# Kernel tuning notes

Measured on AMD Instinct MI355X. Metric: run time of the kernel, lower is better.

The kernel has to match this reference:

```python
import jax, jax.numpy as jnp
import numpy as np
import math

N, E, G, D, H, L = 10000, 160000, 64, 480, 4, 6
DH = D // H          # 120 dims per head
NB = 128             # number of radial basis functions
SH = 9               # 1+3+5 spherical-harmonic channels (l=0,1,2)
CUTOFF = 5.0
AVG_DEG = 15.57930850982666
AVG_NODES = 18.03065905448718


def _silu(x):
    return x * jax.nn.sigmoid(x)


def _sph_harm(vec):
    # component-normalized real spherical harmonics l=0,1,2 on unit vectors
    r = jnp.linalg.norm(vec, axis=-1, keepdims=True) + 1e-12
    u = vec / r
    x, y, z = u[:, 0], u[:, 1], u[:, 2]
    s3, s5, s15 = math.sqrt(3.0), math.sqrt(5.0), math.sqrt(15.0)
    return jnp.stack([
        jnp.ones_like(x),
        s3 * x, s3 * y, s3 * z,
        s15 * x * y, s15 * y * z,
        0.5 * s5 * (3.0 * z * z - 1.0),
        s15 * x * z, 0.5 * s15 * (x * x - y * y)], axis=-1)


def _rbf(d):
    # Gaussian radial basis, centers on [0, cutoff]
    centers = jnp.linspace(0.0, CUTOFF, NB)
    width = CUTOFF / NB
    return jnp.exp(-jnp.square((d[:, None] - centers[None, :]) / width))


def _ln(x):
    mu = jnp.mean(x, axis=-1, keepdims=True)
    var = jnp.var(x, axis=-1, keepdims=True)
    return (x - mu) * jax.lax.rsqrt(var + 1e-5)


def setup_inputs() -> dict:
    key = jax.random.key(0)
    ks = jax.random.split(key, 24)

    def w(k, shape, fan_in):
        return jax.random.normal(k, shape, jnp.float32) / math.sqrt(fan_in)

    inp = {}
    inp["pos"] = jax.random.uniform(ks[0], (N, 3), jnp.float32) * 10.0
    inp["node_atom"] = jax.random.randint(ks[1], (N,), 0, 64)
    inp["edge_src"] = jax.random.randint(ks[2], (E,), 0, N)
    inp["edge_dst"] = jax.random.randint(ks[3], (E,), 0, N)
    inp["batch"] = jnp.sort(jax.random.randint(ks[4], (N,), 0, G))
    # learned parameters
    inp["atom_table"] = w(ks[5], (64, D), 1)
    inp["Wdeg"] = w(ks[6], (SH, D), SH)
    inp["Wd1"] = w(ks[7], (NB, 64), NB)
    inp["Wd2"] = w(ks[8], (64, 64), 64)
    inp["Wd3"] = w(ks[9], (64, 1), 64)
    inp["Wq"] = w(ks[10], (L, D, D), D)
    inp["Wk"] = w(ks[11], (L, D, D), D)
    inp["Wv"] = w(ks[12], (L, D, D), D)
    inp["Wsh"] = w(ks[13], (L, SH, D), SH)
    inp["W1"] = w(ks[14], (L, NB, 64), NB)
    inp["W2"] = w(ks[15], (L, 64, 64), 64)
    inp["W3"] = w(ks[16], (L, 64, H), 64)
    inp["Wo"] = w(ks[17], (L, D, D), D)
    inp["Wf1"] = w(ks[18], (L, D, 2 * D), D)
    inp["Wf2"] = w(ks[19], (L, 2 * D, D), 2 * D)
    inp["Wh1"] = w(ks[20], (D, D), D)
    inp["Wh2"] = w(ks[21], (D, 1), D)
    return inp


def reference(pos, atom_table, Wdeg, Wd1, Wd2, Wd3, Wq, Wk, Wv, Wsh, W1, W2, W3,
              Wo, Wf1, Wf2, Wh1, Wh2, node_atom, edge_src, edge_dst, batch):
    edge_vec = pos[edge_src] - pos[edge_dst]              # [E,3]
    sh = _sph_harm(edge_vec)                              # [E,SH]
    rbf = _rbf(jnp.linalg.norm(edge_vec, axis=-1))        # [E,NB]

    # atom embedding + edge-degree embedding (scatter-sum, rescaled)
    x = atom_table[node_atom]                             # [N,D]
    g0 = _silu(_silu(rbf @ Wd1) @ Wd2) @ Wd3              # [E,1]
    deg = jax.ops.segment_sum((sh @ Wdeg) * g0, edge_dst, num_segments=N)
    x = x + deg / math.sqrt(AVG_DEG)

    inv = 1.0 / math.sqrt(DH)
    for l in range(L):
        # per-edge q/k with SH tensor-product-style mixing and RBF gate
        q = (x @ Wq[l])[edge_dst].reshape(-1, H, DH)
        k = (x[edge_src] @ Wk[l] + sh @ Wsh[l]).reshape(-1, H, DH)
        gate = _silu(_silu(rbf @ W1[l]) @ W2[l]) @ W3[l]  # [E,H]
        logits = jnp.sum(q * k, axis=-1) * inv * gate      # [E,H]
        # per-neighborhood (destination node) softmax
        m = jax.ops.segment_max(logits, edge_dst, num_segments=N)
        a = jnp.exp(logits - m[edge_dst])
        den = jax.ops.segment_sum(a, edge_dst, num_segments=N)
        alpha = a / (den[edge_dst] + 1e-12)                # [E,H]
        v = (x @ Wv[l])[edge_src].reshape(-1, H, DH)
        msg = (alpha[..., None] * v).reshape(-1, D)
        agg = jax.ops.segment_sum(msg, edge_dst, num_segments=N)
        x = _ln(x + (agg / math.sqrt(AVG_DEG)) @ Wo[l])
        x = _ln(x + _silu(x @ Wf1[l]) @ Wf2[l])

    node_e = _silu(x @ Wh1) @ Wh2                          # [N,1]
    energy = jax.ops.segment_sum(node_e[:, 0], batch, num_segments=G) / AVG_NODES
    return energy
```

## Files before the change

### kernel.cpp

```cpp
#include <hip/hip_runtime.h>
#include <hip/hip_bf16.h>

#define NN 10000
#define EE 160000
#define GG 64
#define DD 480
#define HH 4
#define LLAYERS 6
#define DHD 120
#define NB_ 128
#define TSIZE 4096
#define DMAXT 5.5f
#define LSCALE (4095.0f/5.5f)

#define INV_DH 0.09128709291752768f
#define INV_SQRT_DEG 0.25335277f
#define INV_AVG_NODES (1.0f/18.03065905448718f)

typedef __attribute__((ext_vector_type(8))) short bf16x8;
typedef __attribute__((ext_vector_type(4))) float f32x4;
typedef __attribute__((ext_vector_type(8))) unsigned short u16x8;

__device__ __forceinline__ float b2f(unsigned short u){ return __uint_as_float(((unsigned)u)<<16); }
__device__ __forceinline__ unsigned short f2b(float f){
  unsigned u = __float_as_uint(f);
  return (unsigned short)((u + 0x7fffu + ((u>>16)&1u)) >> 16);
}
__device__ __forceinline__ float wsum(float v){
  #pragma unroll
  for (int off=32; off>0; off>>=1) v += __shfl_xor(v, off, 64);
  return v;
}
__device__ __forceinline__ void glds16(const void* g, void* l) {
  __builtin_amdgcn_global_load_lds((const __attribute__((address_space(1))) unsigned int*)g,
                                   (__attribute__((address_space(3))) unsigned int*)l, 16, 0, 0);
}

__global__ __launch_bounds__(256) void zero_kernel(int* __restrict__ cnt, float* __restrict__ out){
  int i = blockIdx.x*256 + threadIdx.x;
  if (i < NN) cnt[i] = 0;
  if (i < GG) out[i] = 0.f;
}

__global__ __launch_bounds__(256) void gather_x_kernel(const float* __restrict__ at,
    const int* __restrict__ atom, float* __restrict__ x){
  const int wid = threadIdx.x >> 6, lane = threadIdx.x & 63;
  for (int n = blockIdx.x*4 + wid; n < NN; n += gridDim.x*4) {
    int a = atom[n];
    if (lane < 60) {
      const float4* src = (const float4*)(at + (size_t)a*DD + lane*8);
      float4* dst = (float4*)(x + (size_t)n*DD + lane*8);
      dst[0] = src[0]; dst[1] = src[1];
    }
  }
}

__global__ __launch_bounds__(256) void edge_geom_kernel(const float* __restrict__ pos,
    const int* __restrict__ esrc, const int* __restrict__ edst,
    float* __restrict__ sh, float* __restrict__ dedge){
  const int e = blockIdx.x*256 + threadIdx.x;
  if (e >= EE) return;
  int s = esrc[e], d = edst[e];
  float vx = pos[s*3+0]-pos[d*3+0];
  float vy = pos[s*3+1]-pos[d*3+1];
  float vz = pos[s*3+2]-pos[d*3+2];
  float rr = sqrtf(vx*vx+vy*vy+vz*vz);
  dedge[e] = rr;
  float r = rr + 1e-12f;
  float x = vx/r, y = vy/r, z = vz/r;
  const float s3 = 1.7320508075688772f;
  const float s5 = 2.23606797749979f;
  const float s15 = 3.872983346207417f;
  float* o = sh + (size_t)e*9;
  o[0] = 1.f;
  o[1] = s3*x; o[2] = s3*y; o[3] = s3*z;
  o[4] = s15*x*y; o[5] = s15*y*z;
  o[6] = 0.5f*s5*(3.f*z*z-1.f);
  o[7] = s15*x*z;
  o[8] = 0.5f*s15*(x*x-y*y);
}

__global__ __launch_bounds__(256) void hist_kernel(const int* __restrict__ edst, int* __restrict__ cnt){
  int e = blockIdx.x*256 + threadIdx.x;
  if (e < EE) atomicAdd(&cnt[edst[e]], 1);
}

__global__ __launch_bounds__(1024) void scan_kernel(const int* __restrict__ cnt,
    int* __restrict__ row_ptr, int* __restrict__ cursor){
  __shared__ int sd[1024];
  __shared__ int s_carry;
  if (threadIdx.x == 0) s_carry = 0;
  __syncthreads();
  for (int base = 0; base < NN; base += 1024) {
    int i = base + threadIdx.x;
    int v = (i < NN) ? cnt[i] : 0;
    sd[threadIdx.x] = v;
    __syncthreads();
    for (int off = 1; off < 1024; off <<= 1) {
      int t = 0;
      if ((int)threadIdx.x >= off) t = sd[threadIdx.x - off];
      __syncthreads();
      sd[threadIdx.x] += t;
      __syncthreads();
    }
    int incl = sd[threadIdx.x];
    int carry = s_carry;
    if (i < NN) { row_ptr[i] = carry + incl - v; cursor[i] = carry + incl - v; }
    __syncthreads();
    if (threadIdx.x == 1023) s_carry = carry + incl;
    __syncthreads();
  }
  if (threadIdx.x == 0) row_ptr[NN] = s_carry;
}

__global__ __launch_bounds__(256) void scatter_kernel(const int* __restrict__ esrc,
    const int* __restrict__ edst, int* __restrict__ cursor,
    int* __restrict__ eid, int* __restrict__ srcs){
  int e = blockIdx.x*256 + threadIdx.x;
  if (e < EE) {
    int n = edst[e];
    int p = atomicAdd(&cursor[n], 1);
    eid[p] = e;
    srcs[p] = esrc[e];
  }
}

__global__ __launch_bounds__(1024) void table_kernel(
    const float* __restrict__ Wd1, const float* __restrict__ Wd2, const float* __restrict__ Wd3,
    const float* __restrict__ W1, const float* __restrict__ W2, const float* __restrict__ W3,
    float* __restrict__ Tg, float* __restrict__ Tl) {
  const int chain = blockIdx.y;
  const float *A1, *A2, *A3; int NC;
  if (chain == 0) { A1 = Wd1; A2 = Wd2; A3 = Wd3; NC = 1; }
  else { int l = chain-1; A1 = W1 + (size_t)l*128*64; A2 = W2 + (size_t)l*64*64; A3 = W3 + (size_t)l*64*4; NC = 4; }
  __shared__ float W1s[128*64];
  __shared__ float W2s[64*64];
  __shared__ float W3s[64*4];
  for (int i = threadIdx.x; i < 128*64; i += 1024) W1s[i] = A1[i];
  for (int i = threadIdx.x; i < 64*64; i += 1024) W2s[i] = A2[i];
  for (int i = threadIdx.x; i < 64*4; i += 1024) W3s[i] = (i < 64*NC) ? A3[i] : 0.f;
  __syncthreads();
  const int wid = threadIdx.x >> 6, lane = threadIdx.x & 63;
  const int t = blockIdx.x*16 + wid;
  const float d = (float)t * (DMAXT/(float)(TSIZE-1));
  float t1 = 0.f;
  #pragma unroll 4
  for (int j = 0; j < 128; ++j) {
    float z = (d - (float)j*(5.0f/127.0f)) * (128.0f/5.0f);
    float f = __expf(-z*z);
    t1 += f * W1s[j*64 + lane];
  }
  t1 = t1 / (1.f + __expf(-t1));
  float t2 = 0.f;
  #pragma unroll 4
  for (int c = 0; c < 64; ++c) {
    float bc = __shfl(t1, c);
    t2 += bc * W2s[c*64 + lane];
  }
  t2 = t2 / (1.f + __expf(-t2));
  if (chain == 0) {
    float o = wsum(t2 * W3s[lane]);
    if (lane == 0) Tg[t] = o;
  } else {
    #pragma unroll
    for (int nc = 0; nc < 4; ++nc) {
      float o = wsum(t2 * W3s[lane*4 + nc]);
      if (lane == 0) Tl[((size_t)(chain-1)*TSIZE + t)*4 + nc] = o;
    }
  }
}

__device__ __forceinline__ float lookup1(const float* __restrict__ Tg, float d) {
  float u = d * LSCALE;
  if (u >= (float)(TSIZE-1)) return 0.f;
  int i = (int)u; float fr = u - (float)i;
  float a = Tg[i], b = Tg[i+1];
  return a + fr*(b-a);
}

__global__ __launch_bounds__(256) void transpose_w_kernel(const float* __restrict__ W,
    __hip_bfloat16* __restrict__ Wt, int K, int N, int Npad,
    long long lstrideW, long long lstrideT) {
  __shared__ float T[32][33];
  const int l = blockIdx.z;
  W  += (size_t)l*lstrideW;
  Wt += (size_t)l*lstrideT;
  const int k0 = blockIdx.y*32, n0 = blockIdx.x*32;
  const int tx = threadIdx.x & 31, ty = threadIdx.x >> 5;
  #pragma unroll
  for (int r = 0; r < 32; r += 8) {
    int k = k0 + ty + r, n = n0 + tx;
    T[ty+r][tx] = (k < K && n < N) ? W[(size_t)k*N + n] : 0.f;
  }
  __syncthreads();
  #pragma unroll
  for (int r = 0; r < 32; r += 8) {
    int n = n0 + ty + r, k = k0 + tx;
    if (n < Npad && k < K)
      ((unsigned short*)Wt)[(size_t)n*K + k] = f2b(T[tx][ty+r]);
  }
}

template<int SILU, int OUT>
__global__ __launch_bounds__(512) void gemm_bf16_kernel(
    const __hip_bfloat16* __restrict__ A, const __hip_bfloat16* __restrict__ Bt,
    float* __restrict__ Cf, __hip_bfloat16* __restrict__ Cb0,
    __hip_bfloat16* __restrict__ Cb1, __hip_bfloat16* __restrict__ Cb2,
    int M, int K, int Nc) {
  __shared__ char smem[16384];
  char* AsB = smem;
  char* BsB = smem + 8192;
  const int tid = threadIdx.x;
  const int lane = tid & 63, wid = tid >> 6;
  const int wm = wid >> 2, wn = wid & 3;
  const long long m0 = (long long)blockIdx.y * 128;
  const int n0 = blockIdx.x * 128;

  const int skhi = wid >> 1, srow = (wid & 1)*64 + lane;
  long long gra = m0 + srow; if (gra >= M) gra = M - 1;
  const __hip_bfloat16* aptr = A + gra * (size_t)K + skhi*8;
  const __hip_bfloat16* bptr = Bt + (size_t)(n0 + srow) * K + skhi*8;
  char* adst = AsB + (skhi*128 + srow)*16;
  char* bdst = BsB + (skhi*128 + srow)*16;

  f32x4 acc[4][2];
  #pragma unroll
  for (int i = 0; i < 4; ++i)
    #pragma unroll
    for (int j = 0; j < 2; ++j)
      acc[i][j] = (f32x4){0.f,0.f,0.f,0.f};

  const int lr = lane & 15, lkh = lane >> 4;

  for (int kt = 0; kt < K; kt += 32) {
    __syncthreads();
    glds16(aptr + kt, adst);
    glds16(bptr + kt, bdst);
    __syncthreads();
    bf16x8 afr[4], bfr[2];
    #pragma unroll
    for (int fm = 0; fm < 4; ++fm)
      afr[fm] = *reinterpret_cast<const bf16x8*>(AsB + (lkh*128 + wm*64 + fm*16 + lr)*16);
    #pragma unroll
    for (int fn = 0; fn < 2; ++fn)
      bfr[fn] = *reinterpret_cast<const bf16x8*>(BsB + (lkh*128 + wn*32 + fn*16 + lr)*16);
    #pragma unroll
    for (int fm = 0; fm < 4; ++fm)
      #pragma unroll
      for (int fn = 0; fn < 2; ++fn)
        acc[fm][fn] = __builtin_amdgcn_mfma_f32_16x16x32_bf16(afr[fm], bfr[fn], acc[fm][fn], 0, 0, 0);
  }

  const int seg = n0 >> 9;
  const int c0 = (OUT == 2) ? (n0 & 511) : n0;
  unsigned short* qdst = nullptr;
  if (OUT == 2) qdst = (unsigned short*)(seg == 0 ? Cb0 : (seg == 1 ? Cb1 : Cb2));
  #pragma unroll
  for (int fm = 0; fm < 4; ++fm) {
    #pragma unroll
    for (int fn = 0; fn < 2; ++fn) {
      #pragma unroll
      for (int j = 0; j < 4; ++j) {
        long long r = m0 + wm*64 + fm*16 + lkh*4 + j;
        int c = c0 + wn*32 + fn*16 + lr;
        if (r < M && c < Nc) {
          float v = acc[fm][fn][j];
          if (SILU) v = v / (1.f + __expf(-v));
          if (OUT == 0) Cf[r*(size_t)Nc + c] = v;
          else if (OUT == 1) ((unsigned short*)Cb0)[r*(size_t)Nc + c] = f2b(v);
          else qdst[r*(size_t)Nc + c] = f2b(v);
        }
      }
    }
  }
}

__global__ __launch_bounds__(256) void deg_kernel(const float* __restrict__ dedge,
    const float* __restrict__ sh, const float* __restrict__ Tg,
    const int* __restrict__ row_ptr, const int* __restrict__ eid,
    const float* __restrict__ Wdeg, float* __restrict__ x, __hip_bfloat16* __restrict__ xb) {
  const int wid = threadIdx.x >> 6, lane = threadIdx.x & 63;
  for (int n = blockIdx.x*4 + wid; n < NN; n += gridDim.x*4) {
    const int e0 = row_ptr[n], e1 = row_ptr[n+1];
    float s9[9] = {0,0,0,0,0,0,0,0,0};
    for (int p = e0 + lane; p < e1; p += 64) {
      int e = eid[p];
      float g = lookup1(Tg, dedge[e]);
      const float* srow = sh + (size_t)e*9;
      #pragma unroll
      for (int s = 0; s < 9; ++s) s9[s] += g*srow[s];
    }
    #pragma unroll
    for (int s = 0; s < 9; ++s) s9[s] = wsum(s9[s]);
    #pragma unroll
    for (int r = 0; r < 8; ++r) {
      int d = lane + (r<<6);
      if (d < DD) {
        float acc = 0.f;
        #pragma unroll
        for (int s = 0; s < 9; ++s) acc += s9[s]*Wdeg[s*DD + d];
        float vv = x[(size_t)n*DD + d] + acc * INV_SQRT_DEG;
        x[(size_t)n*DD + d] = vv;
        ((unsigned short*)xb)[(size_t)n*DD + d] = f2b(vv);
      }
    }
  }
}

__global__ __launch_bounds__(256) void p_kernel(const __hip_bfloat16* __restrict__ xq,
    const float* __restrict__ Wsh_l, float* __restrict__ P) {
  const int wid = threadIdx.x >> 6, lane = threadIdx.x & 63;
  for (int n = blockIdx.x*4 + wid; n < NN; n += gridDim.x*4) {
    if (lane < 36) {
      int h = lane/9, s = lane%9;
      const unsigned short* q = (const unsigned short*)(xq + (size_t)n*DD + h*DHD);
      const float* w = Wsh_l + s*DD + h*DHD;
      float acc = 0.f;
      #pragma unroll
      for (int db = 0; db < 15; ++db) {
        u16x8 v = *reinterpret_cast<const u16x8*>(q + db*8);
        #pragma unroll
        for (int j = 0; j < 8; ++j) acc += b2f(v[j])*w[db*8+j];
      }
      P[(size_t)n*36 + lane] = acc;
    }
  }
}

__global__ __launch_bounds__(256) void coef_kernel(
    const int* __restrict__ eid, const int* __restrict__ edst,
    const float* __restrict__ sh, const float* __restrict__ dedge,
    const float* __restrict__ Tl, const float* __restrict__ P,
    float2* __restrict__ sb) {
  const int p = blockIdx.x*256 + threadIdx.x;
  if (p >= EE) return;
  const int e = eid[p];
  const int n = edst[e];
  const float* srow = sh + (size_t)e*9;
  float s0 = srow[0], s1 = srow[1], s2 = srow[2], s3 = srow[3], s4 = srow[4];
  float s5 = srow[5], s6 = srow[6], s7 = srow[7], s8 = srow[8];
  const float* Pn = P + (size_t)n*36;
  float g[4];
  {
    float u = dedge[e] * LSCALE;
    if (u >= (float)(TSIZE-1)) { g[0]=g[1]=g[2]=g[3]=0.f; }
    else {
      int ti = (int)u; float fr = u - (float)ti;
      const float4 ga = *reinterpret_cast<const float4*>(Tl + ti*4);
      const float4 gb = *reinterpret_cast<const float4*>(Tl + ti*4 + 4);
      g[0] = ga.x + fr*(gb.x-ga.x); g[1] = ga.y + fr*(gb.y-ga.y);
      g[2] = ga.z + fr*(gb.z-ga.z); g[3] = ga.w + fr*(gb.w-ga.w);
    }
  }
  #pragma unroll
  for (int h = 0; h < 4; ++h) {
    const float* Ph = Pn + h*9;
    float lp = s0*Ph[0]+s1*Ph[1]+s2*Ph[2]+s3*Ph[3]+s4*Ph[4]
             + s5*Ph[5]+s6*Ph[6]+s7*Ph[7]+s8*Ph[8];
    float sc = INV_DH * g[h];
    sb[(size_t)p*4 + h] = make_float2(sc, lp*sc);
  }
}

__global__ __launch_bounds__(256) void attn_kernel(
    const __hip_bfloat16* __restrict__ xq, const __hip_bfloat16* __restrict__ xk,
    const __hip_bfloat16* __restrict__ xv, const float2* __restrict__ sb,
    const int* __restrict__ row_ptr, const int* __restrict__ srcs,
    __hip_bfloat16* __restrict__ aggout) {
  const int wid = threadIdx.x >> 6, lane = threadIdx.x & 63;
  __shared__ float l_s[4][64][4];
  __shared__ int   src_sh[4][64];
  float (*ls)[4] = l_s[wid];
  int* srcS = src_sh[wid];
  const int hh = lane >> 4, li = lane & 15;
  const int hd = (lane < 60) ? (lane/15) : 3;
  const unsigned short* xkp = (const unsigned short*)xk;
  const unsigned short* xvp = (const unsigned short*)xv;
  const int doff = hh*DHD + li*8;
  for (int n = blockIdx.x*4 + wid; n < NN; n += gridDim.x*4) {
    const int e0 = row_ptr[n], e1 = row_ptr[n+1];
    float qf[8] = {0,0,0,0,0,0,0,0};
    if (li < 15) {
      u16x8 v = *reinterpret_cast<const u16x8*>((const unsigned short*)xq + (size_t)n*DD + doff);
      #pragma unroll
      for (int j = 0; j < 8; ++j) qf[j] = b2f(v[j]);
    }
    float m_reg = -1e30f, den_reg = 0.f;
    float agg[8] = {0,0,0,0,0,0,0,0};
    for (int c0 = e0; c0 < e1; c0 += 64) {
      const int cn = min(64, e1 - c0);
      if (lane < cn) srcS[lane] = srcs[c0 + lane];
      asm volatile("s_waitcnt lgkmcnt(0)" ::: "memory");
      int i = 0;
      for (; i + 4 <= cn; i += 4) {
        int sA = srcS[i], sB = srcS[i+1], sC = srcS[i+2], sD = srcS[i+3];
        float a0 = 0.f, a1 = 0.f, a2 = 0.f, a3 = 0.f;
        if (li < 15) {
          u16x8 k0 = *reinterpret_cast<const u16x8*>(xkp + (size_t)sA*DD + doff);
          u16x8 k1 = *reinterpret_cast<const u16x8*>(xkp + (size_t)sB*DD + doff);
          u16x8 k2 = *reinterpret_cast<const u16x8*>(xkp + (size_t)sC*DD + doff);
          u16x8 k3 = *reinterpret_cast<const u16x8*>(xkp + (size_t)sD*DD + doff);
          #pragma unroll
          for (int j = 0; j < 8; ++j) {
            a0 += qf[j]*b2f(k0[j]);
            a1 += qf[j]*b2f(k1[j]);
            a2 += qf[j]*b2f(k2[j]);
            a3 += qf[j]*b2f(k3[j]);
          }
        }
        #pragma unroll
        for (int off = 1; off < 16; off <<= 1) {
          a0 += __shfl_xor(a0, off, 64);
          a1 += __shfl_xor(a1, off, 64);
          a2 += __shfl_xor(a2, off, 64);
          a3 += __shfl_xor(a3, off, 64);
        }
        if (li == 0) {
          float2 cA = sb[(size_t)(c0+i+0)*4 + hh];
          float2 cB = sb[(size_t)(c0+i+1)*4 + hh];
          float2 cC = sb[(size_t)(c0+i+2)*4 + hh];
          float2 cD = sb[(size_t)(c0+i+3)*4 + hh];
          ls[i+0][hh] = a0*cA.x + cA.y;
          ls[i+1][hh] = a1*cB.x + cB.y;
          ls[i+2][hh] = a2*cC.x + cC.y;
          ls[i+3][hh] = a3*cD.x + cD.y;
        }
      }
      for (; i < cn; ++i) {
        int sA = srcS[i];
        float a0 = 0.f;
        if (li < 15) {
          u16x8 k0 = *reinterpret_cast<const u16x8*>(xkp + (size_t)sA*DD + doff);
          #pragma unroll
          for (int j = 0; j < 8; ++j) a0 += qf[j]*b2f(k0[j]);
        }
        #pragma unroll
        for (int off = 1; off < 16; off <<= 1) a0 += __shfl_xor(a0, off, 64);
        if (li == 0) {
          float2 cA = sb[(size_t)(c0+i)*4 + hh];
          ls[i][hh] = a0*cA.x + cA.y;
        }
      }
      asm volatile("s_waitcnt lgkmcnt(0)" ::: "memory");
      const int h = lane & 3, i0 = lane >> 2;
      float cm = -1e30f;
      for (int i2 = i0; i2 < cn; i2 += 16) cm = fmaxf(cm, ls[i2][h]);
      #pragma unroll
      for (int off = 4; off < 64; off <<= 1) cm = fmaxf(cm, __shfl_xor(cm, off, 64));
      const float newm = fmaxf(m_reg, cm);
      const float f = __expf(m_reg - newm);
      float cs = 0.f;
      for (int i2 = i0; i2 < cn; i2 += 16) {
        float a = __expf(ls[i2][h] - newm);
        ls[i2][h] = a;
        cs += a;
      }
      #pragma unroll
      for (int off = 4; off < 64; off <<= 1) cs += __shfl_xor(cs, off, 64);
      m_reg = newm;
      den_reg = den_reg*f + cs;
      asm volatile("s_waitcnt lgkmcnt(0)" ::: "memory");
      const float fh = __shfl(f, hd);
      #pragma unroll
      for (int j = 0; j < 8; ++j) agg[j] *= fh;
      i = 0;
      for (; i + 4 <= cn; i += 4) {
        int sA = srcS[i], sB = srcS[i+1], sC = srcS[i+2], sD = srcS[i+3];
        float a0 = ls[i][hd], a1 = ls[i+1][hd], a2 = ls[i+2][hd], a3 = ls[i+3][hd];
        if (lane < 60) {
          u16x8 v0 = *reinterpret_cast<const u16x8*>(xvp + (size_t)sA*DD + lane*8);
          u16x8 v1 = *reinterpret_cast<const u16x8*>(xvp + (size_t)sB*DD + lane*8);
          u16x8 v2 = *reinterpret_cast<const u16x8*>(xvp + (size_t)sC*DD + lane*8);
          u16x8 v3 = *reinterpret_cast<const u16x8*>(xvp + (size_t)sD*DD + lane*8);
          #pragma unroll
          for (int j = 0; j < 8; ++j)
            agg[j] += a0*b2f(v0[j]) + a1*b2f(v1[j]) + a2*b2f(v2[j]) + a3*b2f(v3[j]);
        }
      }
      for (; i < cn; ++i) {
        int sA = srcS[i];
        float a0 = ls[i][hd];
        if (lane < 60) {
          u16x8 v0 = *reinterpret_cast<const u16x8*>(xvp + (size_t)sA*DD + lane*8);
          #pragma unroll
          for (int j = 0; j < 8; ++j) agg[j] += a0*b2f(v0[j]);
        }
      }
    }
    const float dh2 = __shfl(den_reg, hd);
    if (lane < 60) {
      const float sc = INV_SQRT_DEG / (dh2 + 1e-12f);
      u16x8 o;
      #pragma unroll
      for (int j = 0; j < 8; ++j) o[j] = f2b(agg[j]*sc);
      *reinterpret_cast<u16x8*>((unsigned short*)aggout + (size_t)n*DD + lane*8) = o;
    }
  }
}

__global__ __launch_bounds__(256) void ln_kernel(float* __restrict__ x, const float* __restrict__ t,
    __hip_bfloat16* __restrict__ xb) {
  const int wid = threadIdx.x >> 6, lane = threadIdx.x & 63;
  for (int n = blockIdx.x*4 + wid; n < NN; n += gridDim.x*4) {
    float4 a0 = make_float4(0,0,0,0), a1 = make_float4(0,0,0,0);
    float s = 0.f, s2 = 0.f;
    if (lane < 60) {
      const float4* xp = (const float4*)(x + (size_t)n*DD + lane*8);
      const float4* tp = (const float4*)(t + (size_t)n*DD + lane*8);
      float4 b0 = tp[0], b1 = tp[1];
      a0 = xp[0]; a1 = xp[1];
      a0.x += b0.x; a0.y += b0.y; a0.z += b0.z; a0.w += b0.w;
      a1.x += b1.x; a1.y += b1.y; a1.z += b1.z; a1.w += b1.w;
      s  = a0.x+a0.y+a0.z+a0.w + a1.x+a1.y+a1.z+a1.w;
      s2 = a0.x*a0.x+a0.y*a0.y+a0.z*a0.z+a0.w*a0.w
         + a1.x*a1.x+a1.y*a1.y+a1.z*a1.z+a1.w*a1.w;
    }
    s = wsum(s); s2 = wsum(s2);
    const float mu = s * (1.f/(float)DD);
    const float var = s2 * (1.f/(float)DD) - mu*mu;
    const float rs = rsqrtf(var + 1e-5f);
    if (lane < 60) {
      float4* xp = (float4*)(x + (size_t)n*DD + lane*8);
      a0.x = (a0.x-mu)*rs; a0.y = (a0.y-mu)*rs; a0.z = (a0.z-mu)*rs; a0.w = (a0.w-mu)*rs;
      a1.x = (a1.x-mu)*rs; a1.y = (a1.y-mu)*rs; a1.z = (a1.z-mu)*rs; a1.w = (a1.w-mu)*rs;
      xp[0] = a0; xp[1] = a1;
      u16x8 o;
      o[0]=f2b(a0.x); o[1]=f2b(a0.y); o[2]=f2b(a0.z); o[3]=f2b(a0.w);
      o[4]=f2b(a1.x); o[5]=f2b(a1.y); o[6]=f2b(a1.z); o[7]=f2b(a1.w);
      *reinterpret_cast<u16x8*>((unsigned short*)xb + (size_t)n*DD + lane*8) = o;
    }
  }
}

__global__ __launch_bounds__(256) void h2_kernel(const float* __restrict__ t,
    const float* __restrict__ Wh2, const int* __restrict__ batch, float* __restrict__ out) {
  __shared__ float part[GG];
  for (int i = threadIdx.x; i < GG; i += 256) part[i] = 0.f;
  __syncthreads();
  const int wid = threadIdx.x >> 6, lane = threadIdx.x & 63;
  const int per_block = (NN + gridDim.x - 1) / gridDim.x;
  const int n0 = blockIdx.x * per_block;
  const int n1 = min(NN, n0 + per_block);
  for (int n = n0 + wid; n < n1; n += 4) {
    float s = 0.f;
    if (lane < 60) {
      const float4* tp = (const float4*)(t + (size_t)n*DD + lane*8);
      const float4* wp = (const float4*)(Wh2 + lane*8);
      float4 t0 = tp[0], t1 = tp[1], w0 = wp[0], w1 = wp[1];
      s = t0.x*w0.x+t0.y*w0.y+t0.z*w0.z+t0.w*w0.w
        + t1.x*w1.x+t1.y*w1.y+t1.z*w1.z+t1.w*w1.w;
    }
    s = wsum(s);
    if (lane == 0) atomicAdd(&part[batch[n]], s * INV_AVG_NODES);
  }
  __syncthreads();
  for (int i = threadIdx.x; i < GG; i += 256) {
    float v = part[i];
    if (v != 0.f) atomicAdd(&out[i], v);
  }
}

extern "C" void kernel_launch(void* const* d_in, const int* in_sizes, int n_in,
                              void* d_out, int out_size, void* d_ws, size_t ws_size,
                              hipStream_t stream) {
  const float* pos        = (const float*)d_in[0];
  const int*   node_atom  = (const int*)  d_in[1];
  const int*   edge_src   = (const int*)  d_in[2];
  const int*   edge_dst   = (const int*)  d_in[3];
  const int*   batch      = (const int*)  d_in[4];
  const float* atom_table = (const float*)d_in[5];
  const float* Wdeg       = (const float*)d_in[6];
  const float* Wd1        = (const float*)d_in[7];
  const float* Wd2        = (const float*)d_in[8];
  const float* Wd3        = (const float*)d_in[9];
  const float* Wq         = (const float*)d_in[10];
  const float* Wk         = (const float*)d_in[11];
  const float* Wv         = (const float*)d_in[12];
  const float* Wsh        = (const float*)d_in[13];
  const float* W1         = (const float*)d_in[14];
  const float* W2         = (const float*)d_in[15];
  const float* W3         = (const float*)d_in[16];
  const float* Wo         = (const float*)d_in[17];
  const float* Wf1        = (const float*)d_in[18];
  const float* Wf2        = (const float*)d_in[19];
  const float* Wh1        = (const float*)d_in[20];
  const float* Wh2        = (const float*)d_in[21];
  float* out = (float*)d_out;
  char*  wsb = (char*)d_ws;

  size_t off = 0;
  auto alloc = [&](size_t bytes) { size_t o = off; off += (bytes + 255) & ~(size_t)255; return o; };
  float*  x      = (float*) (wsb + alloc((size_t)NN*DD*4));
  __hip_bfloat16* xb   = (__hip_bfloat16*)(wsb + alloc((size_t)NN*DD*2));
  __hip_bfloat16* xq   = (__hip_bfloat16*)(wsb + alloc((size_t)NN*DD*2));
  __hip_bfloat16* xk   = (__hip_bfloat16*)(wsb + alloc((size_t)NN*DD*2));
  __hip_bfloat16* xv   = (__hip_bfloat16*)(wsb + alloc((size_t)NN*DD*2));
  float*  shb    = (float*) (wsb + alloc((size_t)EE*9*4));
  float*  dedge  = (float*) (wsb + alloc((size_t)EE*4));
  float*  P      = (float*) (wsb + alloc((size_t)NN*36*4));
  float2* sbuf   = (float2*)(wsb + alloc((size_t)EE*4*8));
  __hip_bfloat16* aggb = (__hip_bfloat16*)(wsb + alloc((size_t)NN*DD*2));
  float*  tmp480 = (float*) (wsb + alloc((size_t)NN*DD*4));
  __hip_bfloat16* tmp960 = (__hip_bfloat16*)(wsb + alloc((size_t)NN*960*2));
  float*  Tg     = (float*) (wsb + alloc((size_t)TSIZE*4));
  float*  Tl     = (float*) (wsb + alloc((size_t)LLAYERS*TSIZE*4*4));
  __hip_bfloat16* Wqkvt = (__hip_bfloat16*)(wsb + alloc((size_t)LLAYERS*1536*480*2));
  __hip_bfloat16* Wot   = (__hip_bfloat16*)(wsb + alloc((size_t)LLAYERS*512*480*2));
  __hip_bfloat16* Wf1t  = (__hip_bfloat16*)(wsb + alloc((size_t)LLAYERS*1024*480*2));
  __hip_bfloat16* Wf2t  = (__hip_bfloat16*)(wsb + alloc((size_t)LLAYERS*512*960*2));
  __hip_bfloat16* Wh1t  = (__hip_bfloat16*)(wsb + alloc((size_t)512*480*2));
  int* cnt     = (int*)(wsb + alloc((size_t)NN*4));
  int* row_ptr = (int*)(wsb + alloc((size_t)(NN+1)*4));
  int* cursor  = (int*)(wsb + alloc((size_t)NN*4));
  int* eid     = (int*)(wsb + alloc((size_t)EE*4));
  int* srcs    = (int*)(wsb + alloc((size_t)EE*4));
  (void)ws_size;

  auto tr = [&](const float* W, __hip_bfloat16* Wt, int K, int N, int Npad,
                long long lsW, long long lsT, int L) {
    dim3 g((Npad+31)/32, (K+31)/32, L);
    transpose_w_kernel<<<g, 256, 0, stream>>>(W, Wt, K, N, Npad, lsW, lsT);
  };

  tr(Wq,  Wqkvt + 0*512*480,    480, 480, 512, 480*480, 1536*480, LLAYERS);
  tr(Wk,  Wqkvt + 1*512*480,    480, 480, 512, 480*480, 1536*480, LLAYERS);
  tr(Wv,  Wqkvt + 2*512*480,    480, 480, 512, 480*480, 1536*480, LLAYERS);
  tr(Wo,  Wot,  480, 480, 512, 480*480, 512*480, LLAYERS);
  tr(Wf1, Wf1t, 480, 960, 1024, 480*960, 1024*480, LLAYERS);
  tr(Wf2, Wf2t, 960, 480, 512, 960*480, 512*960, LLAYERS);
  tr(Wh1, Wh1t, 480, 480, 512, 480*480, 512*480, 1);

  zero_kernel<<<(NN+255)/256, 256, 0, stream>>>(cnt, out);
  gather_x_kernel<<<640, 256, 0, stream>>>(atom_table, node_atom, x);
  edge_geom_kernel<<<(EE+255)/256, 256, 0, stream>>>(pos, edge_src, edge_dst, shb, dedge);
  hist_kernel<<<(EE+255)/256, 256, 0, stream>>>(edge_dst, cnt);
  scan_kernel<<<1, 1024, 0, stream>>>(cnt, row_ptr, cursor);
  scatter_kernel<<<(EE+255)/256, 256, 0, stream>>>(edge_src, edge_dst, cursor, eid, srcs);
  table_kernel<<<dim3(TSIZE/16, 1+LLAYERS), 1024, 0, stream>>>(Wd1, Wd2, Wd3, W1, W2, W3, Tg, Tl);
  deg_kernel<<<2500, 256, 0, stream>>>(dedge, shb, Tg, row_ptr, eid, Wdeg, x, xb);

  for (int l = 0; l < LLAYERS; ++l) {
    const __hip_bfloat16* Wqkvt_l = Wqkvt + (size_t)l*1536*480;
    const __hip_bfloat16* Wot_l   = Wot   + (size_t)l*512*480;
    const __hip_bfloat16* Wf1t_l  = Wf1t  + (size_t)l*1024*480;
    const __hip_bfloat16* Wf2t_l  = Wf2t  + (size_t)l*512*960;
    const float* Wsh_l = Wsh + (size_t)l*9*DD;
    const float* Tl_l  = Tl  + (size_t)l*TSIZE*4;

    gemm_bf16_kernel<0,2><<<dim3(12, 79), 512, 0, stream>>>(xb, Wqkvt_l, nullptr, xq, xk, xv, NN, 480, 480);
    p_kernel<<<2500, 256, 0, stream>>>(xq, Wsh_l, P);
    coef_kernel<<<(EE+255)/256, 256, 0, stream>>>(eid, edge_dst, shb, dedge, Tl_l, P, sbuf);
    attn_kernel<<<2500, 256, 0, stream>>>(xq, xk, xv, sbuf, row_ptr, srcs, aggb);
    gemm_bf16_kernel<0,0><<<dim3(4, 79), 512, 0, stream>>>(aggb, Wot_l, tmp480, nullptr, nullptr, nullptr, NN, 480, 480);
    ln_kernel<<<640, 256, 0, stream>>>(x, tmp480, xb);
    gemm_bf16_kernel<1,1><<<dim3(8, 79), 512, 0, stream>>>(xb, Wf1t_l, nullptr, tmp960, nullptr, nullptr, NN, 480, 960);
    gemm_bf16_kernel<0,0><<<dim3(4, 79), 512, 0, stream>>>(tmp960, Wf2t_l, tmp480, nullptr, nullptr, nullptr, NN, 960, 480);
    ln_kernel<<<640, 256, 0, stream>>>(x, tmp480, xb);
  }

  gemm_bf16_kernel<1,0><<<dim3(4, 79), 512, 0, stream>>>(xb, Wh1t, tmp480, nullptr, nullptr, nullptr, NN, 480, 480);
  h2_kernel<<<160, 256, 0, stream>>>(tmp480, Wh2, batch, out);
}
```

Baseline: 1.734 ms.

## Double-buffer GEMM LDS tiles and truncate RBF table loop to nearby centers

The bf16 GEMM now uses two LDS buffers so the next K-tile's global-to-LDS load is issued before the MFMAs on the current tile, with a single waitcnt and barrier per iteration instead of two barriers. This is meant to hide global load latency behind the matrix math, at the cost of doubling shared memory per block, which may lower occupancy. Separately, the radial table build now sums only the 17 Gaussian centers nearest each distance rather than all 128, skipping terms that are negligible. That truncation changes the table values very slightly.

New measurement: 1.726 ms. No clear change (-0.5%).

```diff
diff --git a/kernel.cpp b/kernel.cpp
--- a/kernel.cpp
+++ b/kernel.cpp
@@ -143,10 +143,13 @@
   const int wid = threadIdx.x >> 6, lane = threadIdx.x & 63;
   const int t = blockIdx.x*16 + wid;
   const float d = (float)t * (DMAXT/(float)(TSIZE-1));
+  const float cstep = 5.0f/127.0f;
+  int jc = (int)(d / cstep + 0.5f);
+  int j0 = jc - 8; if (j0 < 0) j0 = 0;
+  int j1 = jc + 8; if (j1 > 127) j1 = 127;
   float t1 = 0.f;
-  #pragma unroll 4
-  for (int j = 0; j < 128; ++j) {
-    float z = (d - (float)j*(5.0f/127.0f)) * (128.0f/5.0f);
+  for (int j = j0; j <= j1; ++j) {
+    float z = (d - (float)j*cstep) * (128.0f/5.0f);
     float f = __expf(-z*z);
     t1 += f * W1s[j*64 + lane];
   }
@@ -207,9 +210,7 @@
     float* __restrict__ Cf, __hip_bfloat16* __restrict__ Cb0,
     __hip_bfloat16* __restrict__ Cb1, __hip_bfloat16* __restrict__ Cb2,
     int M, int K, int Nc) {
-  __shared__ char smem[16384];
-  char* AsB = smem;
-  char* BsB = smem + 8192;
+  __shared__ char smem[32768];
   const int tid = threadIdx.x;
   const int lane = tid & 63, wid = tid >> 6;
   const int wm = wid >> 2, wn = wid & 3;
@@ -220,8 +221,7 @@
   long long gra = m0 + srow; if (gra >= M) gra = M - 1;
   const __hip_bfloat16* aptr = A + gra * (size_t)K + skhi*8;
   const __hip_bfloat16* bptr = Bt + (size_t)(n0 + srow) * K + skhi*8;
-  char* adst = AsB + (skhi*128 + srow)*16;
-  char* bdst = BsB + (skhi*128 + srow)*16;
+  const int stoff = (skhi*128 + srow)*16;
 
   f32x4 acc[4][2];
   #pragma unroll
@@ -232,11 +232,19 @@
 
   const int lr = lane & 15, lkh = lane >> 4;
 
+  glds16(aptr, smem + stoff);
+  glds16(bptr, smem + 8192 + stoff);
+  __syncthreads();
+
+  int cur = 0;
   for (int kt = 0; kt < K; kt += 32) {
-    __syncthreads();
-    glds16(aptr + kt, adst);
-    glds16(bptr + kt, bdst);
-    __syncthreads();
+    const int nxt = cur ^ 1;
+    if (kt + 32 < K) {
+      glds16(aptr + kt + 32, smem + nxt*16384 + stoff);
+      glds16(bptr + kt + 32, smem + nxt*16384 + 8192 + stoff);
+    }
+    const char* AsB = smem + cur*16384;
+    const char* BsB = AsB + 8192;
     bf16x8 afr[4], bfr[2];
     #pragma unroll
     for (int fm = 0; fm < 4; ++fm)
@@ -249,6 +257,9 @@
       #pragma unroll
       for (int fn = 0; fn < 2; ++fn)
         acc[fm][fn] = __builtin_amdgcn_mfma_f32_16x16x32_bf16(afr[fm], bfr[fn], acc[fm][fn], 0, 0, 0);
+    asm volatile("s_waitcnt vmcnt(0)" ::: "memory");
+    asm volatile("s_barrier" ::: "memory");
+    cur = nxt;
   }
 
   const int seg = n0 >> 9;
```
